# Kernel optimization log

Measured on AMD Instinct MI355X. Metric: run time of the kernel, lower is better.

The kernel has to match this reference:

```python
import jax, jax.numpy as jnp
import numpy as np

N = 1024
BATCH = 16384


def setup_inputs() -> dict:
    key = jax.random.key(0)
    k1, k2 = jax.random.split(key)
    log_alpha = jax.random.normal(k1, (BATCH, N), dtype=jnp.float32)
    W = jax.random.normal(k2, (N, N), dtype=jnp.float32)  # unnormalized_transition_matrix
    return {"log_alpha": log_alpha, "W": W}


def reference(log_alpha, W):
    # log_softmax over dim=0 (columns sum to 1 in prob space)
    logT = jax.nn.log_softmax(W, axis=0)  # [N, N]
    # log-domain matmul: out[b, i] = logsumexp_k( logT[i, k] + log_alpha[b, k] )
    # Stable exp-shift trick avoids materializing the [B, N, N] broadcast tensor:
    mA = jnp.max(logT, axis=1, keepdims=True)        # [N, 1] row max of logT
    mB = jnp.max(log_alpha, axis=1, keepdims=True)   # [B, 1] row max of log_alpha
    expA = jnp.exp(logT - mA)                        # [N, N]
    expB = jnp.exp(log_alpha - mB)                   # [B, N]
    s = jnp.einsum('bk,ik->bi', expB, expA)          # [B, N]
    return jnp.log(s) + mB + mA.T                    # [B, N]
```

## Files before the change

kernel.cpp:

```cpp
#include <hip/hip_runtime.h>
#include <hip/hip_bf16.h>
#include <stdint.h>

#define MB_ 16384
#define NN_ 1024
#define KK_ 1024

typedef __bf16 bhalf;
typedef __bf16 bhalf8 __attribute__((ext_vector_type(8)));
typedef __bf16 bhalf4 __attribute__((ext_vector_type(4)));
typedef float f32x4 __attribute__((ext_vector_type(4)));

typedef const __attribute__((address_space(1))) void* gas_ptr;
typedef __attribute__((address_space(3))) void* las_ptr;

__device__ __forceinline__ void gload_lds16(const void* g, void* l) {
  __builtin_amdgcn_global_load_lds((gas_ptr)g, (las_ptr)l, 16, 0, 0);
}

__global__ void k_colpart(const float* __restrict__ W,
                          float* __restrict__ pM, float* __restrict__ pS) {
  int col = blockIdx.x * 256 + threadIdx.x;
  int rc  = blockIdx.y;
  const float* p = W + (size_t)rc * 32 * NN_ + col;
  float v[32];
#pragma unroll
  for (int i = 0; i < 32; ++i) v[i] = p[(size_t)i * NN_];
  float m = v[0];
#pragma unroll
  for (int i = 1; i < 32; ++i) m = fmaxf(m, v[i]);
  float s = 0.f;
#pragma unroll
  for (int i = 0; i < 32; ++i) s += __expf(v[i] - m);
  pM[rc * NN_ + col] = m;
  pS[rc * NN_ + col] = s;
}

__global__ void k_colfin(const float* __restrict__ pM, const float* __restrict__ pS,
                         float* __restrict__ colLSE) {
  int col = blockIdx.x * 256 + threadIdx.x;
  float m = -1e30f;
#pragma unroll
  for (int i = 0; i < 32; ++i) m = fmaxf(m, pM[i * NN_ + col]);
  float s = 0.f;
#pragma unroll
  for (int i = 0; i < 32; ++i) s += pS[i * NN_ + col] * __expf(pM[i * NN_ + col] - m);
  colLSE[col] = m + __logf(s);
}

__global__ void k_expA(const float* __restrict__ W, const float* __restrict__ colLSE,
                       bhalf* __restrict__ eA, float* __restrict__ mA) {
  int i = blockIdx.x;
  int l = threadIdx.x;
  const float4* row = (const float4*)(W + (size_t)i * NN_);
  const float4* cls = (const float4*)colLSE;
  float4 v[4];
#pragma unroll
  for (int t = 0; t < 4; ++t) {
    float4 wv = row[t * 64 + l];
    float4 cv = cls[t * 64 + l];
    v[t].x = wv.x - cv.x; v[t].y = wv.y - cv.y;
    v[t].z = wv.z - cv.z; v[t].w = wv.w - cv.w;
  }
  float m = -1e30f;
#pragma unroll
  for (int t = 0; t < 4; ++t)
    m = fmaxf(m, fmaxf(fmaxf(v[t].x, v[t].y), fmaxf(v[t].z, v[t].w)));
#pragma unroll
  for (int off = 32; off; off >>= 1) m = fmaxf(m, __shfl_xor(m, off));
#pragma unroll
  for (int t = 0; t < 4; ++t) {
    bhalf4 o;
    o[0] = (bhalf)__expf(v[t].x - m);
    o[1] = (bhalf)__expf(v[t].y - m);
    o[2] = (bhalf)__expf(v[t].z - m);
    o[3] = (bhalf)__expf(v[t].w - m);
    *(bhalf4*)(eA + (size_t)i * NN_ + t * 256 + l * 4) = o;
  }
  if (l == 0) mA[i] = m;
}

__global__ void k_expB(const float* __restrict__ LA,
                       bhalf* __restrict__ eB, float* __restrict__ mB) {
  int b = blockIdx.x;
  int l = threadIdx.x;
  const float4* row = (const float4*)(LA + (size_t)b * NN_);
  float4 v[4];
#pragma unroll
  for (int t = 0; t < 4; ++t) v[t] = row[t * 64 + l];
  float m = -1e30f;
#pragma unroll
  for (int t = 0; t < 4; ++t)
    m = fmaxf(m, fmaxf(fmaxf(v[t].x, v[t].y), fmaxf(v[t].z, v[t].w)));
#pragma unroll
  for (int off = 32; off; off >>= 1) m = fmaxf(m, __shfl_xor(m, off));
#pragma unroll
  for (int t = 0; t < 4; ++t) {
    bhalf4 o;
    o[0] = (bhalf)__expf(v[t].x - m);
    o[1] = (bhalf)__expf(v[t].y - m);
    o[2] = (bhalf)__expf(v[t].z - m);
    o[3] = (bhalf)__expf(v[t].w - m);
    *(bhalf4*)(eB + (size_t)b * NN_ + t * 256 + l * 4) = o;
  }
  if (l == 0) mB[b] = m;
}

__global__ __launch_bounds__(512, 2) void k_gemm(const bhalf* __restrict__ A,
                                                 const bhalf* __restrict__ Bt,
                                                 const float* __restrict__ mB,
                                                 const float* __restrict__ mA,
                                                 float* __restrict__ out) {
  __shared__ __align__(16) unsigned char lds[131072];

  const int nwg = gridDim.x;
  const int wg  = blockIdx.x;
  const int swz = (wg & 7) * (nwg >> 3) + (wg >> 3);
  const int bm = swz >> 2;
  const int bn = swz & 3;

  const int tid = threadIdx.x;
  const int l = tid & 63;
  const int w = tid >> 6;
  const int wr = w >> 2;
  const int wc = w & 3;

  const int r8  = tid >> 3;
  const int kel = (((tid & 7) ^ (r8 & 7)) << 3);
  const bhalf* A_blk = A  + (size_t)(bm * 256) * KK_;
  const bhalf* B_blk = Bt + (size_t)(bn * 256) * KK_;

  auto stA = [&](int t, int h) {
    unsigned char* dst = lds + (t & 1) * 65536 + h * 16384 + tid * 16;
    const bhalf* g = A_blk + (size_t)(h * 128 + r8) * KK_ + t * 64 + kel;
    gload_lds16(g, dst);
    gload_lds16(g + (size_t)64 * KK_, dst + 8192);
  };
  auto stB = [&](int t, int h) {
    unsigned char* dst = lds + (t & 1) * 65536 + 32768 + h * 16384 + tid * 16;
    const bhalf* g = B_blk + (size_t)(h * 128 + r8) * KK_ + t * 64 + kel;
    gload_lds16(g, dst);
    gload_lds16(g + (size_t)64 * KK_, dst + 8192);
  };

  const int kx  = 16 * (l >> 4);
  const int x16 = (l & 7) << 4;

  f32x4 zero = {0.f, 0.f, 0.f, 0.f};
  f32x4 acc[8][4];
#pragma unroll
  for (int m = 0; m < 8; ++m)
#pragma unroll
    for (int n = 0; n < 4; ++n) acc[m][n] = zero;

  stA(0, 0); stA(0, 1);
  stB(0, 0); stB(0, 1);
  stB(1, 0); stB(1, 1);
  asm volatile("s_waitcnt vmcnt(4)" ::: "memory");
  __builtin_amdgcn_s_barrier();

  const int NT = KK_ / 64;
  for (int t = 0; t < NT; ++t) {
    unsigned char* sAb = lds + (t & 1) * 65536;
    unsigned char* sBb = sAb + 32768;
    bhalf8 bq[4][2];
#pragma unroll
    for (int q = 0; q < 4; ++q) {
      bhalf8 af[2][2];
#pragma unroll
      for (int m = 0; m < 2; ++m) {
        const int row = wr * 128 + q * 32 + m * 16 + (l & 15);
#pragma unroll
        for (int kk = 0; kk < 2; ++kk)
          af[m][kk] = *(const bhalf8*)(sAb + row * 128 + ((kk * 64 + kx) ^ x16));
      }
      if (q == 0) {
#pragma unroll
        for (int n = 0; n < 4; ++n) {
          const int row = wc * 64 + n * 16 + (l & 15);
#pragma unroll
          for (int kk = 0; kk < 2; ++kk)
            bq[n][kk] = *(const bhalf8*)(sBb + row * 128 + ((kk * 64 + kx) ^ x16));
        }
      }
      if (q == 0)      stA(t + 1 < NT ? t + 1 : NT - 1, 0);
      else if (q == 1) stA(t + 1 < NT ? t + 1 : NT - 1, 1);
      else if (q == 2) stB(t + 2 < NT ? t + 2 : NT - 1, 0);
      else             stB(t + 2 < NT ? t + 2 : NT - 1, 1);

      if (q == 3) asm volatile("s_waitcnt vmcnt(4)" ::: "memory");
      __builtin_amdgcn_s_barrier();
      asm volatile("s_waitcnt lgkmcnt(0)" ::: "memory");
      __builtin_amdgcn_sched_barrier(0);
      __builtin_amdgcn_s_setprio(1);
#pragma unroll
      for (int m = 0; m < 2; ++m)
#pragma unroll
        for (int n = 0; n < 4; ++n)
#pragma unroll
          for (int kk = 0; kk < 2; ++kk)
            acc[2 * q + m][n] =
                __builtin_amdgcn_mfma_f32_16x16x32_bf16(af[m][kk], bq[n][kk], acc[2 * q + m][n], 0, 0, 0);
      __builtin_amdgcn_s_setprio(0);
      __builtin_amdgcn_s_barrier();
    }
  }

  const int c0 = bn * 256 + wc * 64 + (l & 15);
  const int r0 = bm * 256 + wr * 128 + (l >> 4) * 4;
  float mav[4];
#pragma unroll
  for (int nf = 0; nf < 4; ++nf) mav[nf] = mA[c0 + nf * 16];
#pragma unroll
  for (int mf = 0; mf < 8; ++mf) {
#pragma unroll
    for (int r = 0; r < 4; ++r) {
      const int row = r0 + mf * 16 + r;
      const float mb = mB[row];
      float* o = out + (size_t)row * NN_ + c0;
#pragma unroll
      for (int nf = 0; nf < 4; ++nf)
        o[nf * 16] = __logf(acc[mf][nf][r]) + mb + mav[nf];
    }
  }
}

extern "C" void kernel_launch(void* const* d_in, const int* in_sizes, int n_in,
                              void* d_out, int out_size, void* d_ws, size_t ws_size,
                              hipStream_t stream) {
  const float* log_alpha = (const float*)d_in[0];
  const float* W         = (const float*)d_in[1];
  float* out = (float*)d_out;

  uintptr_t ws = (uintptr_t)d_ws;
  bhalf* eB     = (bhalf*)(ws);
  bhalf* eA     = (bhalf*)(ws + 33554432);
  float* mB     = (float*)(ws + 35651584);
  float* mA     = (float*)(ws + 35717120);
  float* colLSE = (float*)(ws + 35721216);
  float* pM     = (float*)(ws + 35725312);
  float* pS     = (float*)(ws + 35856384);

  k_colpart<<<dim3(4, 32), 256, 0, stream>>>(W, pM, pS);
  k_colfin<<<4, 256, 0, stream>>>(pM, pS, colLSE);
  k_expA<<<NN_, 64, 0, stream>>>(W, colLSE, eA, mA);
  k_expB<<<MB_, 64, 0, stream>>>(log_alpha, eB, mB);
  k_gemm<<<(MB_ / 256) * (NN_ / 256), 512, 0, stream>>>(eB, eA, mB, mA, out);
}
```

Baseline: 69.53 us.

## Manually unroll GEMM K-loop with macro phases and precomputed LDS pointers

Rewrites the GEMM main loop as explicit two-tile macro-expanded stages. Global and LDS addresses are precomputed once, and the clamped redundant loads in the final tiles are replaced with an explicit epilogue that drains with vmcnt(0). It also adds an lgkmcnt hint before the barrier and switches output writes to nontemporal stores. The goals are less address arithmetic, no wasted tail loads and less cache pollution from the output. In exchange the code is more complex and more fragile with respect to waitcnt correctness.

```diff
diff --git a/kernel.cpp b/kernel.cpp
--- a/kernel.cpp
+++ b/kernel.cpp
@@ -106,6 +106,65 @@
   if (l == 0) mB[b] = m;
 }
 
+
+#define VM4   asm volatile("s_waitcnt vmcnt(4)" ::: "memory")
+#define VM0   asm volatile("s_waitcnt vmcnt(0)" ::: "memory")
+#define HINT8 asm volatile("s_waitcnt lgkmcnt(8)" ::: "memory")
+#define NOPS  ((void)0)
+
+#define STA(BUF, H, TOFF) do {                                            \
+    const bhalf* g_ = pgA + (H) * 131072 + (TOFF) * 64;                   \
+    unsigned char* d_ = lds + (BUF) * 32768 + (H) * 16384 + tid * 16;     \
+    gload_lds16(g_, d_); gload_lds16(g_ + 65536, d_ + 8192); } while (0)
+
+#define STB(BUF, H, TOFF) do {                                            \
+    const bhalf* g_ = pgB + (H) * 131072 + (TOFF) * 64;                   \
+    unsigned char* d_ = lds + 65536 + (BUF) * 32768 + (H) * 16384 + tid * 16; \
+    gload_lds16(g_, d_); gload_lds16(g_ + 65536, d_ + 8192); } while (0)
+
+#define MFMA8(Q)                                                          \
+  __builtin_amdgcn_s_setprio(1);                                          \
+  _Pragma("unroll")                                                       \
+  for (int m_ = 0; m_ < 2; ++m_)                                          \
+    _Pragma("unroll")                                                     \
+    for (int n_ = 0; n_ < 4; ++n_)                                        \
+      _Pragma("unroll")                                                   \
+      for (int kk_ = 0; kk_ < 2; ++kk_)                                   \
+        acc[2 * (Q) + m_][n_] = __builtin_amdgcn_mfma_f32_16x16x32_bf16(  \
+            af[m_][kk_], bq[n_][kk_], acc[2 * (Q) + m_][n_], 0, 0, 0);    \
+  __builtin_amdgcn_s_setprio(0);
+
+#define PHASE(BUF, Q, STG, PRE)                                           \
+  af[0][0] = *(const bhalf8*)(pA0 + (BUF) * 32768 + (Q) * 4096);          \
+  af[0][1] = *(const bhalf8*)(pA1 + (BUF) * 32768 + (Q) * 4096);          \
+  af[1][0] = *(const bhalf8*)(pA0 + (BUF) * 32768 + (Q) * 4096 + 2048);   \
+  af[1][1] = *(const bhalf8*)(pA1 + (BUF) * 32768 + (Q) * 4096 + 2048);   \
+  if ((Q) == 0) {                                                         \
+    _Pragma("unroll")                                                     \
+    for (int n_ = 0; n_ < 4; ++n_) {                                      \
+      bq[n_][0] = *(const bhalf8*)(pB0 + (BUF) * 32768 + n_ * 2048);      \
+      bq[n_][1] = *(const bhalf8*)(pB1 + (BUF) * 32768 + n_ * 2048);      \
+    }                                                                     \
+  }                                                                       \
+  STG;                                                                    \
+  PRE;                                                                    \
+  __builtin_amdgcn_sched_barrier(0);                                      \
+  __builtin_amdgcn_s_barrier();                                           \
+  asm volatile("s_waitcnt lgkmcnt(0)" ::: "memory");                      \
+  __builtin_amdgcn_sched_barrier(0);                                      \
+  MFMA8(Q);                                                               \
+  __builtin_amdgcn_s_barrier();
+
+#define KTILE(BUF, S0, S1, S2, S3, PRE0, PRE3)                            \
+  {                                                                       \
+    bhalf8 bq[4][2];                                                      \
+    bhalf8 af[2][2];                                                      \
+    PHASE(BUF, 0, S0, PRE0)                                               \
+    PHASE(BUF, 1, S1, NOPS)                                               \
+    PHASE(BUF, 2, S2, NOPS)                                               \
+    PHASE(BUF, 3, S3, PRE3)                                               \
+  }
+
 __global__ __launch_bounds__(512, 2) void k_gemm(const bhalf* __restrict__ A,
                                                  const bhalf* __restrict__ Bt,
                                                  const float* __restrict__ mB,
@@ -127,24 +186,17 @@
 
   const int r8  = tid >> 3;
   const int kel = (((tid & 7) ^ (r8 & 7)) << 3);
-  const bhalf* A_blk = A  + (size_t)(bm * 256) * KK_;
-  const bhalf* B_blk = Bt + (size_t)(bn * 256) * KK_;
-
-  auto stA = [&](int t, int h) {
-    unsigned char* dst = lds + (t & 1) * 65536 + h * 16384 + tid * 16;
-    const bhalf* g = A_blk + (size_t)(h * 128 + r8) * KK_ + t * 64 + kel;
-    gload_lds16(g, dst);
-    gload_lds16(g + (size_t)64 * KK_, dst + 8192);
-  };
-  auto stB = [&](int t, int h) {
-    unsigned char* dst = lds + (t & 1) * 65536 + 32768 + h * 16384 + tid * 16;
-    const bhalf* g = B_blk + (size_t)(h * 128 + r8) * KK_ + t * 64 + kel;
-    gload_lds16(g, dst);
-    gload_lds16(g + (size_t)64 * KK_, dst + 8192);
-  };
+  const bhalf* pgA = A  + (size_t)(bm * 256 + r8) * KK_ + kel;
+  const bhalf* pgB = Bt + (size_t)(bn * 256 + r8) * KK_ + kel;
 
   const int kx  = 16 * (l >> 4);
   const int x16 = (l & 7) << 4;
+  const int kx0 = kx ^ x16;
+  const int kx1 = (64 + kx) ^ x16;
+  const unsigned char* pA0 = lds + wr * 16384 + (l & 15) * 128 + kx0;
+  const unsigned char* pA1 = lds + wr * 16384 + (l & 15) * 128 + kx1;
+  const unsigned char* pB0 = lds + 65536 + (wc >> 1) * 16384 + ((wc & 1) * 64 + (l & 15)) * 128 + kx0;
+  const unsigned char* pB1 = lds + 65536 + (wc >> 1) * 16384 + ((wc & 1) * 64 + (l & 15)) * 128 + kx1;
 
   f32x4 zero = {0.f, 0.f, 0.f, 0.f};
   f32x4 acc[8][4];
@@ -153,58 +205,20 @@
 #pragma unroll
     for (int n = 0; n < 4; ++n) acc[m][n] = zero;
 
-  stA(0, 0); stA(0, 1);
-  stB(0, 0); stB(0, 1);
-  stB(1, 0); stB(1, 1);
-  asm volatile("s_waitcnt vmcnt(4)" ::: "memory");
+  STA(0, 0, 0); STA(0, 1, 0);
+  STB(0, 0, 0); STB(0, 1, 0);
+  STB(1, 0, 1); STB(1, 1, 1);
+  VM4;
   __builtin_amdgcn_s_barrier();
 
-  const int NT = KK_ / 64;
-  for (int t = 0; t < NT; ++t) {
-    unsigned char* sAb = lds + (t & 1) * 65536;
-    unsigned char* sBb = sAb + 32768;
-    bhalf8 bq[4][2];
-#pragma unroll
-    for (int q = 0; q < 4; ++q) {
-      bhalf8 af[2][2];
-#pragma unroll
-      for (int m = 0; m < 2; ++m) {
-        const int row = wr * 128 + q * 32 + m * 16 + (l & 15);
-#pragma unroll
-        for (int kk = 0; kk < 2; ++kk)
-          af[m][kk] = *(const bhalf8*)(sAb + row * 128 + ((kk * 64 + kx) ^ x16));
-      }
-      if (q == 0) {
-#pragma unroll
-        for (int n = 0; n < 4; ++n) {
-          const int row = wc * 64 + n * 16 + (l & 15);
-#pragma unroll
-          for (int kk = 0; kk < 2; ++kk)
-            bq[n][kk] = *(const bhalf8*)(sBb + row * 128 + ((kk * 64 + kx) ^ x16));
-        }
-      }
-      if (q == 0)      stA(t + 1 < NT ? t + 1 : NT - 1, 0);
-      else if (q == 1) stA(t + 1 < NT ? t + 1 : NT - 1, 1);
-      else if (q == 2) stB(t + 2 < NT ? t + 2 : NT - 1, 0);
-      else             stB(t + 2 < NT ? t + 2 : NT - 1, 1);
-
-      if (q == 3) asm volatile("s_waitcnt vmcnt(4)" ::: "memory");
-      __builtin_amdgcn_s_barrier();
-      asm volatile("s_waitcnt lgkmcnt(0)" ::: "memory");
-      __builtin_amdgcn_sched_barrier(0);
-      __builtin_amdgcn_s_setprio(1);
-#pragma unroll
-      for (int m = 0; m < 2; ++m)
-#pragma unroll
-        for (int n = 0; n < 4; ++n)
-#pragma unroll
-          for (int kk = 0; kk < 2; ++kk)
-            acc[2 * q + m][n] =
-                __builtin_amdgcn_mfma_f32_16x16x32_bf16(af[m][kk], bq[n][kk], acc[2 * q + m][n], 0, 0, 0);
-      __builtin_amdgcn_s_setprio(0);
-      __builtin_amdgcn_s_barrier();
-    }
-  }
+  for (int p = 0; p < 7; ++p) {
+    KTILE(0, STA(1, 0, 1), STA(1, 1, 1), STB(0, 0, 2), STB(0, 1, 2), HINT8, VM4)
+    KTILE(1, STA(0, 0, 2), STA(0, 1, 2), STB(1, 0, 3), STB(1, 1, 3), HINT8, VM4)
+    pgA += 128;
+    pgB += 128;
+  }
+  KTILE(0, STA(1, 0, 1), STA(1, 1, 1), NOPS, NOPS, HINT8, VM0)
+  KTILE(1, NOPS, NOPS, NOPS, NOPS, HINT8, NOPS)
 
   const int c0 = bn * 256 + wc * 64 + (l & 15);
   const int r0 = bm * 256 + wr * 128 + (l >> 4) * 4;
@@ -220,7 +234,7 @@
       float* o = out + (size_t)row * NN_ + c0;
 #pragma unroll
       for (int nf = 0; nf < 4; ++nf)
-        o[nf * 16] = __logf(acc[mf][nf][r]) + mb + mav[nf];
+        __builtin_nontemporal_store(__logf(acc[mf][nf][r]) + mb + mav[nf], o + nf * 16);
     }
   }
 }
```

Measured after the change: 73.79 us. +6.1%, slower.
